# Kernel tuning notes

Hardware: AMD Instinct MI355X
Metric: run time of the kernel (lower is better)

The kernel has to match this reference:

```python
import jax, jax.numpy as jnp
import numpy as np

N, E = 50000, 800000
H, C, K = 8, 16, 4
LAMBD = 1.0
DECAY = [float(np.log(LAMBD / (k + 1) + (1 + 1e-06))) for k in range(K + 1)]


def setup_inputs() -> dict:
    key = jax.random.key(0)
    ks = jax.random.split(key, 10)
    s = 0.05  # keep activations stable over K hops
    return {
        "x": jax.random.normal(ks[0], (N, 256), jnp.float32),
        "edge_index": jax.random.randint(ks[1], (2, E), 0, N, jnp.int64),
        "W0": jax.random.normal(ks[2], (256, 128), jnp.float32) * s,
        "b0": jnp.zeros((128,), jnp.float32),
        "W1": jax.random.normal(ks[3], (128, 128), jnp.float32) * s,
        "b1": jnp.zeros((128,), jnp.float32),
        "Wout": jax.random.normal(ks[4], (128, 40), jnp.float32) * s,
        "bout": jnp.zeros((40,), jnp.float32),
        "hop_att0": jax.random.normal(ks[5], (H, C), jnp.float32) * s,
        "hop_atts": jax.random.normal(ks[6], (K, H, 2 * C), jnp.float32) * s,
        "atts": jax.random.normal(ks[7], (K, H, C), jnp.float32) * s,
        "hop_biases": jnp.ones((K + 1, H), jnp.float32),
    }


def _aero_forward(x, edge_index, W0, b0, W1, b1, Wout, bout,
                  hop_att0, hop_atts, atts, hop_biases):
    n = x.shape[0]
    # add self loops (cached_edge_index is None in the torch module)
    loops = jnp.arange(n, dtype=edge_index.dtype)
    row = jnp.concatenate([edge_index[0], loops])  # source j
    col = jnp.concatenate([edge_index[1], loops])  # target i

    # hid_feat_init (dropout p=0 -> identity); num_layers=2
    h = x @ W0 + b0
    h = jax.nn.elu(h) @ W1 + b1
    h = h.reshape(n, H, C)

    # k = 0 hop attention
    g = jnp.einsum('hc,nhc->nh', hop_att0, jax.nn.elu(h)) + hop_biases[0]
    z = h * g[..., None]
    z_scale = z * DECAY[0]

    for k in range(1, K + 1):
        # edge attention: gather, elementwise, degree-normalize
        zi = z_scale[col]          # [E', H, C] target
        zj = z_scale[row]          # [E', H, C] source
        a = jnp.einsum('hc,ehc->eh', atts[k - 1], jax.nn.elu(zi + zj))
        a = jax.nn.softplus(a) + 1e-06                       # [E', H]
        deg = jax.ops.segment_sum(a, col, num_segments=n)    # [N, H]
        dinv = jnp.where(deg > 0, deg ** -0.5, 0.0)
        a = dinv[row] * a * dinv[col]
        # propagate: scatter-add weighted source features onto targets
        h = jax.ops.segment_sum(a[..., None] * h[row], col, num_segments=n)
        # hop attention on concat(h, z_scale)
        hz = jax.nn.elu(jnp.concatenate([h, z_scale], axis=-1))  # [N, H, 2C]
        g = jnp.einsum('hc,nhc->nh', hop_atts[k - 1], hz) + hop_biases[k]
        z = z + h * g[..., None]
        z_scale = z * DECAY[k]

    # node classifier
    z = jax.nn.elu(z.reshape(n, H * C))
    return z @ Wout + bout


def reference(x, edge_index, W0, b0, W1, b1, Wout, bout,
              hop_att0, hop_atts, atts, hop_biases):
    return _aero_forward(x, edge_index, W0, b0, W1, b1, Wout, bout,
                         hop_att0, hop_atts, atts, hop_biases)
```

## Files before the change

### kernel.cpp

```cpp
#include <hip/hip_runtime.h>
#include <hip/hip_fp16.h>
#include <math.h>

#define NH 8
#define NC 16
#define HC 128

typedef __attribute__((ext_vector_type(4))) _Float16 half4;

__device__ __forceinline__ float eluf(float x) { return x > 0.f ? x : __expf(x) - 1.f; }
__device__ __forceinline__ float splusf(float x) { return fmaxf(x, 0.f) + __logf(1.f + __expf(-fabsf(x))); }

__global__ void count_kernel(const int* __restrict__ ei, int* __restrict__ cnt, int E, int E2) {
    int e = blockIdx.x * blockDim.x + threadIdx.x;
    if (e >= E2) return;
    int col = (e < E) ? ei[E + e] : (e - E);
    atomicAdd(&cnt[col], 1);
}

__global__ void scan1_kernel(const int* __restrict__ counts, int* __restrict__ ptr,
                             int* __restrict__ partials, int n) {
    __shared__ int tmp[256];
    int t = threadIdx.x;
    int i = blockIdx.x * 256 + t;
    int v = (i < n) ? counts[i] : 0;
    tmp[t] = v;
    __syncthreads();
    for (int off = 1; off < 256; off <<= 1) {
        int add = (t >= off) ? tmp[t - off] : 0;
        __syncthreads();
        tmp[t] += add;
        __syncthreads();
    }
    if (i < n) ptr[i] = tmp[t] - v;
    if (t == 255) partials[blockIdx.x] = tmp[255];
}

__global__ void scan2_kernel(int* __restrict__ partials, int nb) {
    __shared__ int tmp[256];
    int t = threadIdx.x;
    int v = (t < nb) ? partials[t] : 0;
    tmp[t] = v;
    __syncthreads();
    for (int off = 1; off < 256; off <<= 1) {
        int add = (t >= off) ? tmp[t - off] : 0;
        __syncthreads();
        tmp[t] += add;
        __syncthreads();
    }
    if (t < nb) partials[t] = tmp[t] - v;
}

__global__ void scan3_kernel(int* __restrict__ ptr, const int* __restrict__ partials,
                             int n, int total) {
    int i = blockIdx.x * 256 + threadIdx.x;
    if (i < n) ptr[i] += partials[blockIdx.x];
    if (i == 0) ptr[n] = total;
}

__global__ void fill_kernel(const int* __restrict__ ei, const int* __restrict__ ptr,
                            int* __restrict__ cursor, int* __restrict__ src, int E, int E2) {
    int e = blockIdx.x * blockDim.x + threadIdx.x;
    if (e >= E2) return;
    int col, row;
    if (e < E) { row = ei[e]; col = ei[E + e]; }
    else       { row = e - E; col = e - E; }
    int pos = ptr[col] + atomicAdd(&cursor[col], 1);
    src[pos] = row;
}

template<int K, bool ELU_OUT, bool HOP0>
__global__ __launch_bounds__(256)
void mlp_gemm(const float* __restrict__ A, const float* __restrict__ W,
              const float* __restrict__ bias, float* __restrict__ out, int M,
              float* __restrict__ z_out, _Float16* __restrict__ h16_out,
              const float* __restrict__ att0, const float* __restrict__ hb0) {
    __shared__ float As[16][132];
    __shared__ float Ws[16][128];
    const int tid = threadIdx.x;
    const int m0 = blockIdx.x * 128;
    const int tm = tid >> 4;
    const int tn = tid & 15;
    float acc[8][8];
#pragma unroll
    for (int i = 0; i < 8; ++i)
#pragma unroll
        for (int j = 0; j < 8; ++j) acc[i][j] = 0.f;

    const int ra = tid >> 1;
    const int ha = (tid & 1) * 8;
    const int rw = tid >> 4;
    const int cw = (tid & 15) * 8;

    for (int k0 = 0; k0 < K; k0 += 16) {
        float4 a0 = make_float4(0.f, 0.f, 0.f, 0.f), a1 = a0;
        int garow = m0 + ra;
        if (garow < M) {
            const float* ap = A + (size_t)garow * K + k0 + ha;
            a0 = *(const float4*)(ap);
            a1 = *(const float4*)(ap + 4);
        }
        const float* wp = W + (size_t)(k0 + rw) * 128 + cw;
        float4 w0 = *(const float4*)(wp);
        float4 w1 = *(const float4*)(wp + 4);
        __syncthreads();
        As[ha + 0][ra] = a0.x; As[ha + 1][ra] = a0.y; As[ha + 2][ra] = a0.z; As[ha + 3][ra] = a0.w;
        As[ha + 4][ra] = a1.x; As[ha + 5][ra] = a1.y; As[ha + 6][ra] = a1.z; As[ha + 7][ra] = a1.w;
        *(float4*)&Ws[rw][cw]     = w0;
        *(float4*)&Ws[rw][cw + 4] = w1;
        __syncthreads();
#pragma unroll
        for (int kk = 0; kk < 16; ++kk) {
            float ar[8], wr[8];
            *(float4*)&ar[0] = *(const float4*)&As[kk][tm * 8];
            *(float4*)&ar[4] = *(const float4*)&As[kk][tm * 8 + 4];
            *(float4*)&wr[0] = *(const float4*)&Ws[kk][tn * 8];
            *(float4*)&wr[4] = *(const float4*)&Ws[kk][tn * 8 + 4];
#pragma unroll
            for (int i = 0; i < 8; ++i)
#pragma unroll
                for (int j = 0; j < 8; ++j)
                    acc[i][j] = fmaf(ar[i], wr[j], acc[i][j]);
        }
    }
#pragma unroll
    for (int i = 0; i < 8; ++i) {
        int r = m0 + tm * 8 + i;
        float vv[8];
#pragma unroll
        for (int j = 0; j < 8; ++j) {
            float v = acc[i][j] + bias[tn * 8 + j];
            if (ELU_OUT) v = eluf(v);
            vv[j] = v;
        }
        if (HOP0) {
            float part = 0.f;
#pragma unroll
            for (int j = 0; j < 8; ++j)
                part += att0[tn * 8 + j] * eluf(vv[j]);
            part += __shfl_xor(part, 1);
            float g = part + hb0[tn >> 1];
            if (r < M) {
                _Float16* hp = h16_out + (size_t)r * 128 + tn * 8;
                float* zp = z_out + (size_t)r * 128 + tn * 8;
                half4 h0, h1;
                h0.x = (_Float16)vv[0]; h0.y = (_Float16)vv[1];
                h0.z = (_Float16)vv[2]; h0.w = (_Float16)vv[3];
                h1.x = (_Float16)vv[4]; h1.y = (_Float16)vv[5];
                h1.z = (_Float16)vv[6]; h1.w = (_Float16)vv[7];
                *(half4*)(hp)     = h0;
                *(half4*)(hp + 4) = h1;
#pragma unroll
                for (int j = 0; j < 8; ++j) zp[j] = vv[j] * g;
            }
        } else {
            if (r < M) {
                float* op = out + (size_t)r * 128 + tn * 8;
#pragma unroll
                for (int j = 0; j < 8; ++j) op[j] = vv[j];
            }
        }
    }
}

__global__ __launch_bounds__(256)
void passA_kernel(const float* __restrict__ z, const int* __restrict__ ptr,
                  const int* __restrict__ src, const float* __restrict__ att,
                  float decay, _Float16* __restrict__ a_e, float* __restrict__ dinv, int n) {
    int wid = (int)((blockIdx.x * 256u + threadIdx.x) >> 6);
    if (wid >= n) return;
    const int lane = threadIdx.x & 63;
    const int half = lane >> 5;
    const int q    = lane & 31;
    const int hd   = q >> 2;
    const unsigned i = (unsigned)wid;

    float4 zi = *(const float4*)(z + (i << 7) + (q << 2));
    zi.x *= decay; zi.y *= decay; zi.z *= decay; zi.w *= decay;
    const float4 av = *(const float4*)(att + (q << 2));

    int s0 = ptr[wid], s1 = ptr[wid + 1];
    float dacc = 0.f;
    int s = s0 + half;
    for (; s + 6 < s1; s += 8) {
        unsigned j0 = (unsigned)src[s];
        unsigned j1 = (unsigned)src[s + 2];
        unsigned j2 = (unsigned)src[s + 4];
        unsigned j3 = (unsigned)src[s + 6];
        const float4 r0 = *(const float4*)(z + (j0 << 7) + (q << 2));
        const float4 r1 = *(const float4*)(z + (j1 << 7) + (q << 2));
        const float4 r2 = *(const float4*)(z + (j2 << 7) + (q << 2));
        const float4 r3 = *(const float4*)(z + (j3 << 7) + (q << 2));
        float p0, p1, p2, p3;
        p0  = av.x * eluf(fmaf(r0.x, decay, zi.x));
        p0 += av.y * eluf(fmaf(r0.y, decay, zi.y));
        p0 += av.z * eluf(fmaf(r0.z, decay, zi.z));
        p0 += av.w * eluf(fmaf(r0.w, decay, zi.w));
        p1  = av.x * eluf(fmaf(r1.x, decay, zi.x));
        p1 += av.y * eluf(fmaf(r1.y, decay, zi.y));
        p1 += av.z * eluf(fmaf(r1.z, decay, zi.z));
        p1 += av.w * eluf(fmaf(r1.w, decay, zi.w));
        p2  = av.x * eluf(fmaf(r2.x, decay, zi.x));
        p2 += av.y * eluf(fmaf(r2.y, decay, zi.y));
        p2 += av.z * eluf(fmaf(r2.z, decay, zi.z));
        p2 += av.w * eluf(fmaf(r2.w, decay, zi.w));
        p3  = av.x * eluf(fmaf(r3.x, decay, zi.x));
        p3 += av.y * eluf(fmaf(r3.y, decay, zi.y));
        p3 += av.z * eluf(fmaf(r3.z, decay, zi.z));
        p3 += av.w * eluf(fmaf(r3.w, decay, zi.w));
        p0 += __shfl_xor(p0, 1); p1 += __shfl_xor(p1, 1);
        p2 += __shfl_xor(p2, 1); p3 += __shfl_xor(p3, 1);
        p0 += __shfl_xor(p0, 2); p1 += __shfl_xor(p1, 2);
        p2 += __shfl_xor(p2, 2); p3 += __shfl_xor(p3, 2);
        if ((q & 3) == 0) {
            float a0 = splusf(p0) + 1e-6f;
            float a1 = splusf(p1) + 1e-6f;
            float a2 = splusf(p2) + 1e-6f;
            float a3 = splusf(p3) + 1e-6f;
            a_e[((unsigned)s << 3) + hd] = (_Float16)a0;
            a_e[((unsigned)(s + 2) << 3) + hd] = (_Float16)a1;
            a_e[((unsigned)(s + 4) << 3) + hd] = (_Float16)a2;
            a_e[((unsigned)(s + 6) << 3) + hd] = (_Float16)a3;
            dacc += (a0 + a1) + (a2 + a3);
        }
    }
    for (; s < s1; s += 2) {
        unsigned j = (unsigned)src[s];
        const float4 r = *(const float4*)(z + (j << 7) + (q << 2));
        float p;
        p  = av.x * eluf(fmaf(r.x, decay, zi.x));
        p += av.y * eluf(fmaf(r.y, decay, zi.y));
        p += av.z * eluf(fmaf(r.z, decay, zi.z));
        p += av.w * eluf(fmaf(r.w, decay, zi.w));
        p += __shfl_xor(p, 1);
        p += __shfl_xor(p, 2);
        if ((q & 3) == 0) {
            float aval = splusf(p) + 1e-6f;
            a_e[((unsigned)s << 3) + hd] = (_Float16)aval;
            dacc += aval;
        }
    }
    dacc += __shfl_xor(dacc, 32);
    if (half == 0 && (q & 3) == 0) {
        dinv[(i << 3) + hd] = (dacc > 0.f) ? (1.f / sqrtf(dacc)) : 0.f;
    }
}

__global__ __launch_bounds__(256)
void passB_kernel(const _Float16* __restrict__ h_in, float* __restrict__ z,
                  const int* __restrict__ ptr, const int* __restrict__ src,
                  const _Float16* __restrict__ a_e, const float* __restrict__ dinv,
                  const float* __restrict__ hatt, const float* __restrict__ hb,
                  float decay, _Float16* __restrict__ h_out, int n, int store_h) {
    int wid = (int)((blockIdx.x * 256u + threadIdx.x) >> 6);
    if (wid >= n) return;
    const int lane = threadIdx.x & 63;
    const int half = lane >> 5;
    const int q    = lane & 31;
    const int hd   = q >> 2;
    const unsigned i = (unsigned)wid;

    const float di = dinv[(i << 3) + hd];
    int s0 = ptr[wid], s1 = ptr[wid + 1];
    float ax = 0.f, ay = 0.f, az = 0.f, aw = 0.f;
    int s = s0 + half;
    for (; s + 6 < s1; s += 8) {
        unsigned j0 = (unsigned)src[s];
        unsigned j1 = (unsigned)src[s + 2];
        unsigned j2 = (unsigned)src[s + 4];
        unsigned j3 = (unsigned)src[s + 6];
        float w0 = (float)a_e[((unsigned)s << 3) + hd]       * dinv[(j0 << 3) + hd];
        float w1 = (float)a_e[((unsigned)(s + 2) << 3) + hd] * dinv[(j1 << 3) + hd];
        float w2 = (float)a_e[((unsigned)(s + 4) << 3) + hd] * dinv[(j2 << 3) + hd];
        float w3 = (float)a_e[((unsigned)(s + 6) << 3) + hd] * dinv[(j3 << 3) + hd];
        const half4 f0 = *(const half4*)(h_in + (j0 << 7) + (q << 2));
        const half4 f1 = *(const half4*)(h_in + (j1 << 7) + (q << 2));
        const half4 f2 = *(const half4*)(h_in + (j2 << 7) + (q << 2));
        const half4 f3 = *(const half4*)(h_in + (j3 << 7) + (q << 2));
        ax = fmaf(w0, (float)f0.x, ax); ay = fmaf(w0, (float)f0.y, ay);
        az = fmaf(w0, (float)f0.z, az); aw = fmaf(w0, (float)f0.w, aw);
        ax = fmaf(w1, (float)f1.x, ax); ay = fmaf(w1, (float)f1.y, ay);
        az = fmaf(w1, (float)f1.z, az); aw = fmaf(w1, (float)f1.w, aw);
        ax = fmaf(w2, (float)f2.x, ax); ay = fmaf(w2, (float)f2.y, ay);
        az = fmaf(w2, (float)f2.z, az); aw = fmaf(w2, (float)f2.w, aw);
        ax = fmaf(w3, (float)f3.x, ax); ay = fmaf(w3, (float)f3.y, ay);
        az = fmaf(w3, (float)f3.z, az); aw = fmaf(w3, (float)f3.w, aw);
    }
    for (; s < s1; s += 2) {
        unsigned j = (unsigned)src[s];
        float w = (float)a_e[((unsigned)s << 3) + hd] * dinv[(j << 3) + hd];
        const half4 f = *(const half4*)(h_in + (j << 7) + (q << 2));
        ax = fmaf(w, (float)f.x, ax); ay = fmaf(w, (float)f.y, ay);
        az = fmaf(w, (float)f.z, az); aw = fmaf(w, (float)f.w, aw);
    }
    ax += __shfl_xor(ax, 32);
    ay += __shfl_xor(ay, 32);
    az += __shfl_xor(az, 32);
    aw += __shfl_xor(aw, 32);

    const float4 hn = make_float4(di * ax, di * ay, di * az, di * aw);
    const float4 zv = *(const float4*)(z + (i << 7) + (q << 2));
    const float* hA = hatt + hd * 32 + ((q & 3) << 2);
    float p;
    p  = hA[0] * eluf(hn.x) + hA[1] * eluf(hn.y)
       + hA[2] * eluf(hn.z) + hA[3] * eluf(hn.w);
    p += hA[16] * eluf(zv.x * decay) + hA[17] * eluf(zv.y * decay)
       + hA[18] * eluf(zv.z * decay) + hA[19] * eluf(zv.w * decay);
    p += __shfl_xor(p, 1);
    p += __shfl_xor(p, 2);
    const float g = p + hb[hd];
    if (half == 0) {
        if (store_h) {
            half4 ho;
            ho.x = (_Float16)hn.x; ho.y = (_Float16)hn.y;
            ho.z = (_Float16)hn.z; ho.w = (_Float16)hn.w;
            *(half4*)(h_out + (i << 7) + (q << 2)) = ho;
        }
        *(float4*)(z + (i << 7) + (q << 2)) =
            make_float4(zv.x + hn.x * g, zv.y + hn.y * g,
                        zv.z + hn.z * g, zv.w + hn.w * g);
    }
}

__global__ __launch_bounds__(256)
void gout_kernel(const float* __restrict__ z, const float* __restrict__ W,
                 const float* __restrict__ bias, float* __restrict__ out, int M) {
    __shared__ float zs[128 * 65];
    __shared__ float ws[128 * 40];
    const int tid = threadIdx.x;
    const int r0 = blockIdx.x * 64;
    for (int idx = tid; idx < 128 * 40; idx += 256) ws[idx] = W[idx];
    const int r = tid >> 2;
    const int q = tid & 3;
    {
        int grow = r0 + r;
#pragma unroll
        for (int t = 0; t < 8; ++t) {
            int k = q * 4 + t * 16;
            float4 v = make_float4(0.f, 0.f, 0.f, 0.f);
            if (grow < M) v = *(const float4*)(z + (size_t)grow * HC + k);
            zs[(k + 0) * 65 + r] = eluf(v.x);
            zs[(k + 1) * 65 + r] = eluf(v.y);
            zs[(k + 2) * 65 + r] = eluf(v.z);
            zs[(k + 3) * 65 + r] = eluf(v.w);
        }
    }
    __syncthreads();
    float acc[10];
#pragma unroll
    for (int j = 0; j < 10; ++j) acc[j] = bias[q * 10 + j];
    for (int k = 0; k < 128; ++k) {
        float zk = zs[k * 65 + r];
#pragma unroll
        for (int j = 0; j < 10; ++j)
            acc[j] = fmaf(zk, ws[k * 40 + q * 10 + j], acc[j]);
    }
    int grow = r0 + r;
    if (grow < M) {
        float* op = out + (size_t)grow * 40 + q * 10;
#pragma unroll
        for (int j = 0; j < 10; ++j) op[j] = acc[j];
    }
}

extern "C" void kernel_launch(void* const* d_in, const int* in_sizes, int n_in,
                              void* d_out, int out_size, void* d_ws, size_t ws_size,
                              hipStream_t stream) {
    (void)n_in; (void)out_size; (void)ws_size;
    const float* x    = (const float*)d_in[0];
    const int*   ei   = (const int*)d_in[1];
    const float* W0   = (const float*)d_in[2];
    const float* b0   = (const float*)d_in[3];
    const float* W1   = (const float*)d_in[4];
    const float* b1   = (const float*)d_in[5];
    const float* Wout = (const float*)d_in[6];
    const float* bout = (const float*)d_in[7];
    const float* att0 = (const float*)d_in[8];
    const float* hatts= (const float*)d_in[9];
    const float* atts = (const float*)d_in[10];
    const float* hb   = (const float*)d_in[11];
    float* out = (float*)d_out;

    const int N  = in_sizes[0] / 256;
    const int E  = in_sizes[1] / 2;
    const int E2 = E + N;

    char* p = (char*)d_ws;
    auto carve = [&](size_t bytes) -> char* {
        char* r = p;
        p += (bytes + 255) & ~(size_t)255;
        return r;
    };
    float*    h1     = (float*)carve((size_t)N * HC * 4);
    _Float16* hbufA  = (_Float16*)carve((size_t)N * HC * 2);
    _Float16* hbufB  = (_Float16*)carve((size_t)N * HC * 2);
    float*    zbuf   = (float*)carve((size_t)N * HC * 4);
    _Float16* a_e    = (_Float16*)carve((size_t)E2 * NH * 2);
    float*    dinvb  = (float*)carve((size_t)N * NH * 4);
    int* csr_ptr   = (int*)carve((size_t)(N + 1) * 4);
    int* csr_src   = (int*)carve((size_t)E2 * 4);
    int* cursor    = (int*)carve((size_t)N * 4);
    int* partials  = (int*)carve(1024 * 4);

    float decay[5];
    for (int k = 0; k <= 4; ++k) decay[k] = (float)log(1.0 / (k + 1) + 1.0 + 1e-6);

    hipMemsetAsync(cursor, 0, (size_t)N * 4, stream);
    int eb = (E2 + 255) / 256;
    int nb = (N + 255) / 256;
    count_kernel<<<eb, 256, 0, stream>>>(ei, cursor, E, E2);
    scan1_kernel<<<nb, 256, 0, stream>>>(cursor, csr_ptr, partials, N);
    scan2_kernel<<<1, 256, 0, stream>>>(partials, nb);
    scan3_kernel<<<nb, 256, 0, stream>>>(csr_ptr, partials, N, E2);
    hipMemsetAsync(cursor, 0, (size_t)N * 4, stream);
    fill_kernel<<<eb, 256, 0, stream>>>(ei, csr_ptr, cursor, csr_src, E, E2);

    int gb = (N + 127) / 128;
    mlp_gemm<256, true , false><<<gb, 256, 0, stream>>>(x,  W0, b0, h1, N,
                                                        nullptr, nullptr, nullptr, nullptr);
    mlp_gemm<128, false, true ><<<gb, 256, 0, stream>>>(h1, W1, b1, nullptr, N,
                                                        zbuf, hbufA, att0, hb);

    _Float16* hin  = hbufA;
    _Float16* hout = hbufB;
    int wb = (N + 3) / 4;
    for (int k = 1; k <= 4; ++k) {
        passA_kernel<<<wb, 256, 0, stream>>>(zbuf, csr_ptr, csr_src,
                                             atts + (size_t)(k - 1) * NH * NC,
                                             decay[k - 1], a_e, dinvb, N);
        passB_kernel<<<wb, 256, 0, stream>>>(hin, zbuf, csr_ptr, csr_src, a_e, dinvb,
                                             hatts + (size_t)(k - 1) * NH * 32,
                                             hb + (size_t)k * NH, decay[k - 1], hout, N,
                                             (k < 4) ? 1 : 0);
        _Float16* t = hin; hin = hout; hout = t;
    }

    gout_kernel<<<(N + 63) / 64, 256, 0, stream>>>(zbuf, Wout, bout, out, N);
}
```

Before: 738.3 us.

## Keep fp16 shadow copy of z for edge attention gathers; shrink GEMM tile

Adds an fp16 shadow buffer of z, written by the hop-0 GEMM epilogue and by passB, so that passA gathers half-precision neighbor rows instead of fp32. This halves the bytes of the dominant random gather in the edge-attention pass. The fp32 z is still kept for accumulation and the classifier. Separately, the MLP GEMM row tile drops from 128 to 64 rows to launch more blocks. The costs are extra fp16 writes, some loss of precision in the attention logits, and less register reuse per thread in the GEMM.

```diff
diff --git a/kernel.cpp b/kernel.cpp
--- a/kernel.cpp
+++ b/kernel.cpp
@@ -74,58 +74,54 @@
 void mlp_gemm(const float* __restrict__ A, const float* __restrict__ W,
               const float* __restrict__ bias, float* __restrict__ out, int M,
               float* __restrict__ z_out, _Float16* __restrict__ h16_out,
+              _Float16* __restrict__ z16_out,
               const float* __restrict__ att0, const float* __restrict__ hb0) {
-    __shared__ float As[16][132];
+    __shared__ float As[16][68];
     __shared__ float Ws[16][128];
     const int tid = threadIdx.x;
-    const int m0 = blockIdx.x * 128;
+    const int m0 = blockIdx.x * 64;
     const int tm = tid >> 4;
     const int tn = tid & 15;
-    float acc[8][8];
-#pragma unroll
-    for (int i = 0; i < 8; ++i)
+    float acc[4][8];
+#pragma unroll
+    for (int i = 0; i < 4; ++i)
 #pragma unroll
         for (int j = 0; j < 8; ++j) acc[i][j] = 0.f;
 
-    const int ra = tid >> 1;
-    const int ha = (tid & 1) * 8;
+    const int ra = tid >> 2;
+    const int qa = (tid & 3) * 4;
     const int rw = tid >> 4;
     const int cw = (tid & 15) * 8;
 
     for (int k0 = 0; k0 < K; k0 += 16) {
-        float4 a0 = make_float4(0.f, 0.f, 0.f, 0.f), a1 = a0;
+        float4 a = make_float4(0.f, 0.f, 0.f, 0.f);
         int garow = m0 + ra;
-        if (garow < M) {
-            const float* ap = A + (size_t)garow * K + k0 + ha;
-            a0 = *(const float4*)(ap);
-            a1 = *(const float4*)(ap + 4);
-        }
+        if (garow < M) a = *(const float4*)(A + (size_t)garow * K + k0 + qa);
         const float* wp = W + (size_t)(k0 + rw) * 128 + cw;
         float4 w0 = *(const float4*)(wp);
         float4 w1 = *(const float4*)(wp + 4);
         __syncthreads();
-        As[ha + 0][ra] = a0.x; As[ha + 1][ra] = a0.y; As[ha + 2][ra] = a0.z; As[ha + 3][ra] = a0.w;
-        As[ha + 4][ra] = a1.x; As[ha + 5][ra] = a1.y; As[ha + 6][ra] = a1.z; As[ha + 7][ra] = a1.w;
+        As[qa + 0][ra] = a.x; As[qa + 1][ra] = a.y;
+        As[qa + 2][ra] = a.z; As[qa + 3][ra] = a.w;
         *(float4*)&Ws[rw][cw]     = w0;
         *(float4*)&Ws[rw][cw + 4] = w1;
         __syncthreads();
 #pragma unroll
         for (int kk = 0; kk < 16; ++kk) {
-            float ar[8], wr[8];
-            *(float4*)&ar[0] = *(const float4*)&As[kk][tm * 8];
-            *(float4*)&ar[4] = *(const float4*)&As[kk][tm * 8 + 4];
+            float ar[4], wr[8];
+            *(float4*)&ar[0] = *(const float4*)&As[kk][tm * 4];
             *(float4*)&wr[0] = *(const float4*)&Ws[kk][tn * 8];
             *(float4*)&wr[4] = *(const float4*)&Ws[kk][tn * 8 + 4];
 #pragma unroll
-            for (int i = 0; i < 8; ++i)
+            for (int i = 0; i < 4; ++i)
 #pragma unroll
                 for (int j = 0; j < 8; ++j)
                     acc[i][j] = fmaf(ar[i], wr[j], acc[i][j]);
         }
     }
 #pragma unroll
-    for (int i = 0; i < 8; ++i) {
-        int r = m0 + tm * 8 + i;
+    for (int i = 0; i < 4; ++i) {
+        int r = m0 + tm * 4 + i;
         float vv[8];
 #pragma unroll
         for (int j = 0; j < 8; ++j) {
@@ -142,16 +138,26 @@
             float g = part + hb0[tn >> 1];
             if (r < M) {
                 _Float16* hp = h16_out + (size_t)r * 128 + tn * 8;
+                _Float16* zhp = z16_out + (size_t)r * 128 + tn * 8;
                 float* zp = z_out + (size_t)r * 128 + tn * 8;
-                half4 h0, h1;
+                half4 h0, h1, zh0, zh1;
                 h0.x = (_Float16)vv[0]; h0.y = (_Float16)vv[1];
                 h0.z = (_Float16)vv[2]; h0.w = (_Float16)vv[3];
                 h1.x = (_Float16)vv[4]; h1.y = (_Float16)vv[5];
                 h1.z = (_Float16)vv[6]; h1.w = (_Float16)vv[7];
                 *(half4*)(hp)     = h0;
                 *(half4*)(hp + 4) = h1;
-#pragma unroll
-                for (int j = 0; j < 8; ++j) zp[j] = vv[j] * g;
+                float zz[8];
+#pragma unroll
+                for (int j = 0; j < 8; ++j) zz[j] = vv[j] * g;
+                zh0.x = (_Float16)zz[0]; zh0.y = (_Float16)zz[1];
+                zh0.z = (_Float16)zz[2]; zh0.w = (_Float16)zz[3];
+                zh1.x = (_Float16)zz[4]; zh1.y = (_Float16)zz[5];
+                zh1.z = (_Float16)zz[6]; zh1.w = (_Float16)zz[7];
+                *(half4*)(zhp)     = zh0;
+                *(half4*)(zhp + 4) = zh1;
+#pragma unroll
+                for (int j = 0; j < 8; ++j) zp[j] = zz[j];
             }
         } else {
             if (r < M) {
@@ -164,7 +170,7 @@
 }
 
 __global__ __launch_bounds__(256)
-void passA_kernel(const float* __restrict__ z, const int* __restrict__ ptr,
+void passA_kernel(const _Float16* __restrict__ z16, const int* __restrict__ ptr,
                   const int* __restrict__ src, const float* __restrict__ att,
                   float decay, _Float16* __restrict__ a_e, float* __restrict__ dinv, int n) {
     int wid = (int)((blockIdx.x * 256u + threadIdx.x) >> 6);
@@ -175,8 +181,10 @@
     const int hd   = q >> 2;
     const unsigned i = (unsigned)wid;
 
-    float4 zi = *(const float4*)(z + (i << 7) + (q << 2));
-    zi.x *= decay; zi.y *= decay; zi.z *= decay; zi.w *= decay;
+    const half4 ziH = *(const half4*)(z16 + (i << 7) + (q << 2));
+    float4 zi;
+    zi.x = (float)ziH.x * decay; zi.y = (float)ziH.y * decay;
+    zi.z = (float)ziH.z * decay; zi.w = (float)ziH.w * decay;
     const float4 av = *(const float4*)(att + (q << 2));
 
     int s0 = ptr[wid], s1 = ptr[wid + 1];
@@ -187,27 +195,27 @@
         unsigned j1 = (unsigned)src[s + 2];
         unsigned j2 = (unsigned)src[s + 4];
         unsigned j3 = (unsigned)src[s + 6];
-        const float4 r0 = *(const float4*)(z + (j0 << 7) + (q << 2));
-        const float4 r1 = *(const float4*)(z + (j1 << 7) + (q << 2));
-        const float4 r2 = *(const float4*)(z + (j2 << 7) + (q << 2));
-        const float4 r3 = *(const float4*)(z + (j3 << 7) + (q << 2));
+        const half4 r0 = *(const half4*)(z16 + (j0 << 7) + (q << 2));
+        const half4 r1 = *(const half4*)(z16 + (j1 << 7) + (q << 2));
+        const half4 r2 = *(const half4*)(z16 + (j2 << 7) + (q << 2));
+        const half4 r3 = *(const half4*)(z16 + (j3 << 7) + (q << 2));
         float p0, p1, p2, p3;
-        p0  = av.x * eluf(fmaf(r0.x, decay, zi.x));
-        p0 += av.y * eluf(fmaf(r0.y, decay, zi.y));
-        p0 += av.z * eluf(fmaf(r0.z, decay, zi.z));
-        p0 += av.w * eluf(fmaf(r0.w, decay, zi.w));
-        p1  = av.x * eluf(fmaf(r1.x, decay, zi.x));
-        p1 += av.y * eluf(fmaf(r1.y, decay, zi.y));
-        p1 += av.z * eluf(fmaf(r1.z, decay, zi.z));
-        p1 += av.w * eluf(fmaf(r1.w, decay, zi.w));
-        p2  = av.x * eluf(fmaf(r2.x, decay, zi.x));
-        p2 += av.y * eluf(fmaf(r2.y, decay, zi.y));
-        p2 += av.z * eluf(fmaf(r2.z, decay, zi.z));
-        p2 += av.w * eluf(fmaf(r2.w, decay, zi.w));
-        p3  = av.x * eluf(fmaf(r3.x, decay, zi.x));
-        p3 += av.y * eluf(fmaf(r3.y, decay, zi.y));
-        p3 += av.z * eluf(fmaf(r3.z, decay, zi.z));
-        p3 += av.w * eluf(fmaf(r3.w, decay, zi.w));
+        p0  = av.x * eluf(fmaf((float)r0.x, decay, zi.x));
+        p0 += av.y * eluf(fmaf((float)r0.y, decay, zi.y));
+        p0 += av.z * eluf(fmaf((float)r0.z, decay, zi.z));
+        p0 += av.w * eluf(fmaf((float)r0.w, decay, zi.w));
+        p1  = av.x * eluf(fmaf((float)r1.x, decay, zi.x));
+        p1 += av.y * eluf(fmaf((float)r1.y, decay, zi.y));
+        p1 += av.z * eluf(fmaf((float)r1.z, decay, zi.z));
+        p1 += av.w * eluf(fmaf((float)r1.w, decay, zi.w));
+        p2  = av.x * eluf(fmaf((float)r2.x, decay, zi.x));
+        p2 += av.y * eluf(fmaf((float)r2.y, decay, zi.y));
+        p2 += av.z * eluf(fmaf((float)r2.z, decay, zi.z));
+        p2 += av.w * eluf(fmaf((float)r2.w, decay, zi.w));
+        p3  = av.x * eluf(fmaf((float)r3.x, decay, zi.x));
+        p3 += av.y * eluf(fmaf((float)r3.y, decay, zi.y));
+        p3 += av.z * eluf(fmaf((float)r3.z, decay, zi.z));
+        p3 += av.w * eluf(fmaf((float)r3.w, decay, zi.w));
         p0 += __shfl_xor(p0, 1); p1 += __shfl_xor(p1, 1);
         p2 += __shfl_xor(p2, 1); p3 += __shfl_xor(p3, 1);
         p0 += __shfl_xor(p0, 2); p1 += __shfl_xor(p1, 2);
@@ -226,12 +234,12 @@
     }
     for (; s < s1; s += 2) {
         unsigned j = (unsigned)src[s];
-        const float4 r = *(const float4*)(z + (j << 7) + (q << 2));
+        const half4 r = *(const half4*)(z16 + (j << 7) + (q << 2));
         float p;
-        p  = av.x * eluf(fmaf(r.x, decay, zi.x));
-        p += av.y * eluf(fmaf(r.y, decay, zi.y));
-        p += av.z * eluf(fmaf(r.z, decay, zi.z));
-        p += av.w * eluf(fmaf(r.w, decay, zi.w));
+        p  = av.x * eluf(fmaf((float)r.x, decay, zi.x));
+        p += av.y * eluf(fmaf((float)r.y, decay, zi.y));
+        p += av.z * eluf(fmaf((float)r.z, decay, zi.z));
+        p += av.w * eluf(fmaf((float)r.w, decay, zi.w));
         p += __shfl_xor(p, 1);
         p += __shfl_xor(p, 2);
         if ((q & 3) == 0) {
@@ -248,6 +256,7 @@
 
 __global__ __launch_bounds__(256)
 void passB_kernel(const _Float16* __restrict__ h_in, float* __restrict__ z,
+                  _Float16* __restrict__ z16,
                   const int* __restrict__ ptr, const int* __restrict__ src,
                   const _Float16* __restrict__ a_e, const float* __restrict__ dinv,
                   const float* __restrict__ hatt, const float* __restrict__ hb,
@@ -310,15 +319,18 @@
     p += __shfl_xor(p, 2);
     const float g = p + hb[hd];
     if (half == 0) {
+        float4 zn = make_float4(zv.x + hn.x * g, zv.y + hn.y * g,
+                                zv.z + hn.z * g, zv.w + hn.w * g);
         if (store_h) {
-            half4 ho;
+            half4 ho, zo;
             ho.x = (_Float16)hn.x; ho.y = (_Float16)hn.y;
             ho.z = (_Float16)hn.z; ho.w = (_Float16)hn.w;
             *(half4*)(h_out + (i << 7) + (q << 2)) = ho;
-        }
-        *(float4*)(z + (i << 7) + (q << 2)) =
-            make_float4(zv.x + hn.x * g, zv.y + hn.y * g,
-                        zv.z + hn.z * g, zv.w + hn.w * g);
+            zo.x = (_Float16)zn.x; zo.y = (_Float16)zn.y;
+            zo.z = (_Float16)zn.z; zo.w = (_Float16)zn.w;
+            *(half4*)(z16 + (i << 7) + (q << 2)) = zo;
+        }
+        *(float4*)(z + (i << 7) + (q << 2)) = zn;
     }
 }
 
@@ -395,6 +407,7 @@
     _Float16* hbufA  = (_Float16*)carve((size_t)N * HC * 2);
     _Float16* hbufB  = (_Float16*)carve((size_t)N * HC * 2);
     float*    zbuf   = (float*)carve((size_t)N * HC * 4);
+    _Float16* z16buf = (_Float16*)carve((size_t)N * HC * 2);
     _Float16* a_e    = (_Float16*)carve((size_t)E2 * NH * 2);
     float*    dinvb  = (float*)carve((size_t)N * NH * 4);
     int* csr_ptr   = (int*)carve((size_t)(N + 1) * 4);
@@ -415,20 +428,22 @@
     hipMemsetAsync(cursor, 0, (size_t)N * 4, stream);
     fill_kernel<<<eb, 256, 0, stream>>>(ei, csr_ptr, cursor, csr_src, E, E2);
 
-    int gb = (N + 127) / 128;
+    int gb = (N + 63) / 64;
     mlp_gemm<256, true , false><<<gb, 256, 0, stream>>>(x,  W0, b0, h1, N,
-                                                        nullptr, nullptr, nullptr, nullptr);
+                                                        nullptr, nullptr, nullptr,
+                                                        nullptr, nullptr);
     mlp_gemm<128, false, true ><<<gb, 256, 0, stream>>>(h1, W1, b1, nullptr, N,
-                                                        zbuf, hbufA, att0, hb);
+                                                        zbuf, hbufA, z16buf, att0, hb);
 
     _Float16* hin  = hbufA;
     _Float16* hout = hbufB;
     int wb = (N + 3) / 4;
     for (int k = 1; k <= 4; ++k) {
-        passA_kernel<<<wb, 256, 0, stream>>>(zbuf, csr_ptr, csr_src,
+        passA_kernel<<<wb, 256, 0, stream>>>(z16buf, csr_ptr, csr_src,
                                              atts + (size_t)(k - 1) * NH * NC,
                                              decay[k - 1], a_e, dinvb, N);
-        passB_kernel<<<wb, 256, 0, stream>>>(hin, zbuf, csr_ptr, csr_src, a_e, dinvb,
+        passB_kernel<<<wb, 256, 0, stream>>>(hin, zbuf, z16buf, csr_ptr, csr_src,
+                                             a_e, dinvb,
                                              hatts + (size_t)(k - 1) * NH * 32,
                                              hb + (size_t)k * NH, decay[k - 1], hout, N,
                                              (k < 4) ? 1 : 0);
```

New measurement: 720.9 us. -2.3%, faster.
